# Performance work log

Hardware: AMD Instinct MI355X
Metric: run time of the kernel (lower is better)

The kernel has to match this reference:

```python
import jax, jax.numpy as jnp
import numpy as np
from jax import lax

K = 3          # kernel size
PAD = 1        # padding
STRIDE = 1     # stride (output spatial == input spatial)


def conv2d(x, w, b, pad):
    y = lax.conv_general_dilated(x, w, (1, 1), [(pad, pad), (pad, pad)],
                                 dimension_numbers=("NCHW", "OIHW", "NCHW"))
    return y + b[None, :, None, None]


def bilinear_sample(img, y, x):
    """img: [B,C,H,W]; y,x: [B,Ho,Wo] float coords. Zero outside borders (torchvision semantics)."""
    B, C, H, W = img.shape
    flat = img.reshape(B, C, H * W)
    y0 = jnp.floor(y)
    x0 = jnp.floor(x)
    dy = y - y0
    dx = x - x0

    def gather(yc, xc):
        valid = (yc >= 0) & (yc <= H - 1) & (xc >= 0) & (xc <= W - 1)
        yi = jnp.clip(yc, 0, H - 1).astype(jnp.int32)
        xi = jnp.clip(xc, 0, W - 1).astype(jnp.int32)
        idx = (yi * W + xi).reshape(B, -1)                      # [B, Ho*Wo]
        g = jax.vmap(lambda f, i: f[:, i])(flat, idx)            # [B, C, Ho*Wo]
        g = g.reshape(B, C, y.shape[1], y.shape[2])
        return g * valid[:, None, :, :].astype(img.dtype)

    w00 = ((1 - dy) * (1 - dx))[:, None]
    w01 = ((1 - dy) * dx)[:, None]
    w10 = (dy * (1 - dx))[:, None]
    w11 = (dy * dx)[:, None]
    return (gather(y0, x0) * w00 + gather(y0, x0 + 1) * w01 +
            gather(y0 + 1, x0) * w10 + gather(y0 + 1, x0 + 1) * w11)


def deform_conv2d(feat, offset, weight, bias):
    """feat: [B,C,H,W]; offset: [B,2*K*K,Ho,Wo]; weight: [O,C,K,K]; bias: [O]."""
    B, C, H, W = feat.shape
    Ho, Wo = offset.shape[2], offset.shape[3]
    hh = jnp.arange(Ho, dtype=feat.dtype) * STRIDE - PAD   # base y of kernel origin
    ww = jnp.arange(Wo, dtype=feat.dtype) * STRIDE - PAD
    out = jnp.zeros((B, weight.shape[0], Ho, Wo), feat.dtype)
    for i in range(K):
        for j in range(K):
            k = i * K + j
            sy = hh[None, :, None] + i + offset[:, 2 * k]        # [B,Ho,Wo]
            sx = ww[None, None, :] + j + offset[:, 2 * k + 1]
            sampled = bilinear_sample(feat, sy, sx)               # [B,C,Ho,Wo]
            out = out + jnp.einsum("bchw,oc->bohw", sampled, weight[:, :, i, j])
    return out + bias[None, :, None, None]


def setup_inputs() -> dict:
    key = jax.random.key(0)
    ks = jax.random.split(key, 8)
    IN_CH, OUT_CH = 3, 64
    B, H, W = 4, 256, 256
    s1 = 1.0 / np.sqrt(IN_CH * K * K)
    s2 = 1.0 / np.sqrt(OUT_CH * K * K)
    return {
        "x": jax.random.normal(ks[0], (B, IN_CH, H, W), jnp.float32),
        "conv_w": jax.random.normal(ks[1], (OUT_CH, IN_CH, K, K), jnp.float32) * s1,
        "conv_b": jax.random.normal(ks[2], (OUT_CH,), jnp.float32) * s1,
        "offset_w": jax.random.normal(ks[3], (2 * K * K, OUT_CH, K, K), jnp.float32) * 0.01,
        "offset_b": jax.random.normal(ks[4], (2 * K * K,), jnp.float32) * 0.01,
        "deform_w": jax.random.normal(ks[5], (OUT_CH, OUT_CH, K, K), jnp.float32) * s2,
        "deform_b": jax.random.normal(ks[6], (OUT_CH,), jnp.float32) * s2,
    }


def reference(x, conv_w, conv_b, offset_w, offset_b, deform_w, deform_b):
    feat = conv2d(x, conv_w, conv_b, pad=1)                    # [B,64,H,W]
    offset = conv2d(feat, offset_w, offset_b, pad=PAD)          # [B,18,H,W]
    return deform_conv2d(feat, offset, deform_w, deform_b)
```

## Files before the change

kernel.cpp:

```cpp
#include <hip/hip_runtime.h>
#include <hip/hip_fp16.h>

#define FEAT_N (4*64*256*256)
#define OFFS_N (4*18*256*256)
#define WTF_N  (576*64)
#define WT2F_N (576*32)
#define WT1F_N (4*64*8)

typedef __attribute__((ext_vector_type(8))) _Float16 half8;
typedef __attribute__((ext_vector_type(4))) float float4v;
typedef __attribute__((ext_vector_type(4))) unsigned uint4v;

__device__ __forceinline__ unsigned short f2h(float f) {
    union { __half h; unsigned short u; } c; c.h = __float2half_rn(f); return c.u;
}
__device__ __forceinline__ __half2 u2h2(unsigned u) {
    union { unsigned u; __half2 h; } c; c.u = u; return c.h;
}
__device__ __forceinline__ unsigned h22u(__half2 h) {
    union { __half2 h; unsigned u; } c; c.h = h; return c.u;
}

__global__ __launch_bounds__(256) void prep_weights(const float* __restrict__ dw,
                                                    const float* __restrict__ ow,
                                                    const float* __restrict__ cw,
                                                    unsigned short* __restrict__ wtf,
                                                    unsigned short* __restrict__ wt2f,
                                                    unsigned short* __restrict__ wt1f) {
    int idx = blockIdx.x * 256 + threadIdx.x;
    if (idx < WTF_N) {
        int j    = idx & 7;
        int lane = (idx >> 3) & 63;
        int nt   = (idx >> 9) & 3;
        int ks   = idx >> 11;
        int k    = ks * 32 + ((lane >> 4) << 3) + j;
        int tap  = k >> 6;
        int ic   = k & 63;
        int n    = nt * 16 + (lane & 15);
        wtf[idx] = f2h(dw[n * 576 + ic * 9 + tap]);
    }
    int i2 = idx - WTF_N;
    if (i2 >= 0 && i2 < WT2F_N) {
        int j    = i2 & 7;
        int lane = (i2 >> 3) & 63;
        int nt   = (i2 >> 9) & 1;
        int ks   = i2 >> 10;
        int k    = ks * 32 + ((lane >> 4) << 3) + j;
        int tap  = k >> 6;
        int ic   = k & 63;
        int n    = nt * 16 + (lane & 15);
        wt2f[i2] = (n < 18) ? f2h(ow[n * 576 + ic * 9 + tap]) : (unsigned short)0;
    }
    int i3 = idx - WTF_N - WT2F_N;
    if (i3 >= 0 && i3 < WT1F_N) {
        int j    = i3 & 7;
        int lane = (i3 >> 3) & 63;
        int nt   = (i3 >> 9) & 3;
        int n    = nt * 16 + (lane & 15);
        int k    = ((lane >> 4) << 3) + j;
        wt1f[i3] = (k < 27) ? f2h(cw[n * 27 + k]) : (unsigned short)0;
    }
}

__global__ __launch_bounds__(256) void conv1_kernel(const float* __restrict__ x,
                                                    const unsigned short* __restrict__ wt1f,
                                                    const float* __restrict__ cb,
                                                    unsigned short* __restrict__ featp) {
    __shared__ unsigned short xs[10 * 264];
    const int tid  = threadIdx.x;
    const int lane = tid & 63;
    const int wave = tid >> 6;
    const int lm   = lane & 15;
    const int quad = lane >> 4;

    const int bx = blockIdx.x;
    const int b  = bx >> 8;
    const int h  = bx & 255;

#pragma unroll
    for (int r = 0; r < 9; r++) {
        const int ic = r / 3, ti = r % 3;
        const int srow = h - 1 + ti;
        const bool rok = (unsigned)srow < 256u;
        const float* xrow = x + ((b * 3 + ic) << 16) + (srow << 8);
        {
            const int c = tid;
            float v = (rok && (unsigned)(c - 1) < 256u) ? xrow[c - 1] : 0.f;
            xs[r * 264 + c] = f2h(v);
        }
        if (tid < 2) {
            const int c = tid + 256;
            float v = (rok && (unsigned)(c - 1) < 256u) ? xrow[c - 1] : 0.f;
            xs[r * 264 + c] = f2h(v);
        }
    }
    xs[9 * 264 + tid] = 0;
    if (tid < 8) xs[9 * 264 + 256 + tid] = 0;
    __syncthreads();

    int off[8];
#pragma unroll
    for (int j = 0; j < 8; j++) {
        const int k = quad * 8 + j;
        const int row = (k < 27) ? (k / 3) : 9;
        const int tj  = (k < 27) ? (k - row * 3) : 0;
        off[j] = row * 264 + tj;
    }

    half8 bw[4];
#pragma unroll
    for (int nt = 0; nt < 4; nt++)
        bw[nt] = *(const half8*)(wt1f + nt * 512 + lane * 8);
    float bias[4];
#pragma unroll
    for (int nt = 0; nt < 4; nt++) bias[nt] = cb[nt * 16 + lm];

    unsigned short* fpx = featp + ((((size_t)b << 16) + (h << 8)) << 6);

#pragma unroll
    for (int mt = 0; mt < 4; mt++) {
        const int px = wave * 64 + mt * 16 + lm;
        union { half8 v; unsigned u[4]; } af;
#pragma unroll
        for (int jj = 0; jj < 4; jj++) {
            unsigned lo = xs[off[2 * jj]     + px];
            unsigned hi = xs[off[2 * jj + 1] + px];
            af.u[jj] = lo | (hi << 16);
        }
        float4v d[4];
#pragma unroll
        for (int nt = 0; nt < 4; nt++)
            d[nt] = __builtin_amdgcn_mfma_f32_16x16x32_f16(af.v, bw[nt], (float4v)0.f, 0, 0, 0);

        const int pxs = wave * 64 + mt * 16 + quad * 4;
#pragma unroll
        for (int r = 0; r < 4; r++) {
            unsigned short* sp = fpx + (size_t)(pxs + r) * 64 + lm;
#pragma unroll
            for (int nt = 0; nt < 4; nt++)
                sp[nt * 16] = f2h(d[nt][r] + bias[nt]);
        }
    }
}

__global__ __launch_bounds__(512, 4) void fused_kernel(const unsigned short* __restrict__ featp,
                                                       const unsigned short* __restrict__ wt2f,
                                                       const float* __restrict__ ob,
                                                       const unsigned short* __restrict__ wtf,
                                                       const float* __restrict__ db,
                                                       float* __restrict__ out) {
    __shared__ __align__(16) unsigned char ring[4 * 132 * 128];
    __shared__ float offl[4][18 * 33];

    const int tid  = threadIdx.x;
    const int lane = tid & 63;
    const int wv   = tid >> 6;
    const int ow   = wv >> 1;
    const int mtb  = wv & 1;
    const int lm   = lane & 15;
    const int quad = lane >> 4;

    const int bx = blockIdx.x;
    const int strip = ((bx & 7) << 8) | (bx >> 3);
    const int wo_base = (strip & 1) << 7;
    const int ho = (strip >> 1) & 255;
    const int b  = strip >> 9;

    const unsigned* fpq = (const unsigned*)featp + ((size_t)b << 21) + quad * 4;
    const int colb = wo_base + ow * 32 + mtb * 16 + lm;
    float* offw = &offl[ow][0];

    const char* gbase = (const char*)featp + (((size_t)b << 16) << 7);

#define STAGE_ROW(R)                                                             \
    {                                                                            \
        const int rr = (R);                                                      \
        if ((unsigned)rr < 256u) {                                               \
            const char* gsrc = gbase + ((size_t)(rr << 8) << 7);                 \
            const unsigned base = (unsigned)((rr & 3) * 16896);                  \
            for (int c = tid; c < 1056; c += 512) {                              \
                const int xsl = c >> 3;                                          \
                const int col = wo_base - 2 + xsl;                               \
                if ((unsigned)col < 256u) {                                      \
                    uint4v v = *(const uint4v*)(gsrc + (((size_t)col) << 7)      \
                                                + ((c & 7) << 4));               \
                    const unsigned by = base + (unsigned)(c << 4);               \
                    *(uint4v*)(ring + (by ^ ((unsigned)((xsl & 7) << 4)))) = v;  \
                }                                                                \
            }                                                                    \
        }                                                                        \
    }

    STAGE_ROW(ho - 2);
    STAGE_ROW(ho - 1);
    STAGE_ROW(ho);
    STAGE_ROW(ho + 1);

    {
        float4v acc1[2];
        acc1[0] = (float4v)0.f; acc1[1] = (float4v)0.f;

        uint4v A[2];

#define C2LOAD(KY, KX, DST)                                                      \
    {                                                                            \
        const int row = ho - 1 + (KY);                                           \
        const bool rok = (unsigned)row < 256u;                                   \
        const int col = colb + (KX) - 1;                                         \
        DST[0] = (uint4v)0;                                                      \
        DST[1] = (uint4v)0;                                                      \
        if (rok && (unsigned)col < 256u) {                                       \
            const unsigned* p = fpq + (((row << 8) + col) << 5);                 \
            DST[0] = *(const uint4v*)p;                                          \
            DST[1] = *(const uint4v*)(p + 16);                                   \
        }                                                                        \
    }

        C2LOAD(0, 0, A);

#pragma unroll
        for (int tap = 0; tap < 9; tap++) {
            half8 bfr[2][2];
            const unsigned short* wp = wt2f + (size_t)(tap * 2) * 1024 + lane * 8;
#pragma unroll
            for (int st = 0; st < 2; st++) {
                bfr[st][0] = *(const half8*)(wp + st * 1024);
                bfr[st][1] = *(const half8*)(wp + st * 1024 + 512);
            }
            uint4v N[2];
            if (tap < 8) {
                const int tn  = tap + 1;
                const int tky = tn / 3;
                const int tkx = tn - 3 * tky;
                C2LOAD(tky, tkx, N);
            }
            {
                union { half8 v; uint4v u; } f0, f1;
                f0.u = A[0]; f1.u = A[1];
                acc1[0] = __builtin_amdgcn_mfma_f32_16x16x32_f16(f0.v, bfr[0][0], acc1[0], 0, 0, 0);
                acc1[1] = __builtin_amdgcn_mfma_f32_16x16x32_f16(f0.v, bfr[0][1], acc1[1], 0, 0, 0);
                acc1[0] = __builtin_amdgcn_mfma_f32_16x16x32_f16(f1.v, bfr[1][0], acc1[0], 0, 0, 0);
                acc1[1] = __builtin_amdgcn_mfma_f32_16x16x32_f16(f1.v, bfr[1][1], acc1[1], 0, 0, 0);
            }
            if (tap < 8) { A[0] = N[0]; A[1] = N[1]; }
        }
#undef C2LOAD

#pragma unroll
        for (int nt = 0; nt < 2; nt++) {
            int oc = nt * 16 + lm;
            if (oc < 18) {
                float bv = ob[oc];
#pragma unroll
                for (int r = 0; r < 4; r++)
                    offw[oc * 33 + mtb * 16 + quad * 4 + r] = acc1[nt][r] + bv;
            }
        }
    }

    __syncthreads();

    const int wo0 = wo_base + ow * 32 + mtb * 16 + lm;

    float4v acc[4];
#pragma unroll
    for (int nt = 0; nt < 4; nt++) acc[nt] = (float4v)0.f;

    union AFU { half8 v; unsigned u[4]; };

#define DOTAP(KY, KX, OY, OX)                                                    \
    {                                                                            \
        float sy = (float)(ho - 1 + (KY)) + (OY);                                \
        float sx = (float)(wo0 - 1 + (KX)) + (OX);                               \
        float y0f = floorf(sy), x0f = floorf(sx);                                \
        float dy = sy - y0f, dx = sx - x0f;                                      \
        int y0 = (int)y0f, x0 = (int)x0f;                                        \
        float wy0 = ((unsigned)y0 < 256u) ? (1.f - dy) : 0.f;                    \
        float wy1 = ((unsigned)(y0 + 1) < 256u) ? dy : 0.f;                      \
        float wx0 = ((unsigned)x0 < 256u) ? (1.f - dx) : 0.f;                    \
        float wx1 = ((unsigned)(x0 + 1) < 256u) ? dx : 0.f;                      \
        int yb0 = y0 < 0 ? 0 : (y0 > 255 ? 255 : y0);                            \
        int yb1 = (y0 + 1) < 0 ? 0 : ((y0 + 1) > 255 ? 255 : (y0 + 1));          \
        int xb0 = x0 < 0 ? 0 : (x0 > 255 ? 255 : x0);                            \
        int xb1 = (x0 + 1) < 0 ? 0 : ((x0 + 1) > 255 ? 255 : (x0 + 1));          \
        __half2 W0 = __float2half2_rn(wy0 * wx0);                                \
        __half2 W1 = __float2half2_rn(wy0 * wx1);                                \
        __half2 W2 = __float2half2_rn(wy1 * wx0);                                \
        __half2 W3 = __float2half2_rn(wy1 * wx1);                                \
        uint4v Gg[4][2];                                                         \
        bool inw = (yb0 >= ho - 2 + (KY)) && (yb1 <= ho + (KY) + 1) &&           \
                   (xb0 >= wo_base - 2) && (xb1 <= wo_base + 129);               \
        if (__all(inw)) {                                                        \
            const int xs0 = xb0 - wo_base + 2, xs1 = xb1 - wo_base + 2;          \
            const unsigned m0 = (unsigned)((xs0 & 7) << 4);                      \
            const unsigned m1 = (unsigned)((xs1 & 7) << 4);                      \
            const unsigned r0b = (unsigned)((yb0 & 3) * 16896 + quad * 16);      \
            const unsigned r1b = (unsigned)((yb1 & 3) * 16896 + quad * 16);      \
            const unsigned a00 = r0b + (unsigned)(xs0 << 7);                     \
            const unsigned a01 = r0b + (unsigned)(xs1 << 7);                     \
            const unsigned a10 = r1b + (unsigned)(xs0 << 7);                     \
            const unsigned a11 = r1b + (unsigned)(xs1 << 7);                     \
            Gg[0][0] = *(const uint4v*)(ring + (a00 ^ m0));                      \
            Gg[0][1] = *(const uint4v*)(ring + ((a00 + 64) ^ m0));               \
            Gg[1][0] = *(const uint4v*)(ring + (a01 ^ m1));                      \
            Gg[1][1] = *(const uint4v*)(ring + ((a01 + 64) ^ m1));               \
            Gg[2][0] = *(const uint4v*)(ring + (a10 ^ m0));                      \
            Gg[2][1] = *(const uint4v*)(ring + ((a10 + 64) ^ m0));               \
            Gg[3][0] = *(const uint4v*)(ring + (a11 ^ m1));                      \
            Gg[3][1] = *(const uint4v*)(ring + ((a11 + 64) ^ m1));               \
        } else {                                                                 \
            const unsigned e00 = ((yb0 << 8) + xb0) << 5;                        \
            const unsigned e01 = ((yb0 << 8) + xb1) << 5;                        \
            const unsigned e10 = ((yb1 << 8) + xb0) << 5;                        \
            const unsigned e11 = ((yb1 << 8) + xb1) << 5;                        \
            Gg[0][0] = *(const uint4v*)(fpq + e00);                              \
            Gg[0][1] = *(const uint4v*)(fpq + e00 + 16);                         \
            Gg[1][0] = *(const uint4v*)(fpq + e01);                              \
            Gg[1][1] = *(const uint4v*)(fpq + e01 + 16);                         \
            Gg[2][0] = *(const uint4v*)(fpq + e10);                              \
            Gg[2][1] = *(const uint4v*)(fpq + e10 + 16);                         \
            Gg[3][0] = *(const uint4v*)(fpq + e11);                              \
            Gg[3][1] = *(const uint4v*)(fpq + e11 + 16);                         \
        }                                                                        \
        AFU af[2];                                                               \
        _Pragma("unroll")                                                        \
        for (int st = 0; st < 2; st++) {                                         \
            _Pragma("unroll")                                                    \
            for (int j = 0; j < 4; j++) {                                        \
                __half2 s = __hmul2(W0, u2h2(Gg[0][st][j]));                     \
                s = __hfma2(W1, u2h2(Gg[1][st][j]), s);                          \
                s = __hfma2(W2, u2h2(Gg[2][st][j]), s);                          \
                s = __hfma2(W3, u2h2(Gg[3][st][j]), s);                          \
                af[st].u[j] = h22u(s);                                           \
            }                                                                    \
        }                                                                        \
        _Pragma("unroll")                                                        \
        for (int nt = 0; nt < 4; nt++)                                           \
            acc[nt] = __builtin_amdgcn_mfma_f32_16x16x32_f16(                    \
                af[0].v, bfr[0][nt], acc[nt], 0, 0, 0);                          \
        _Pragma("unroll")                                                        \
        for (int nt = 0; nt < 4; nt++)                                           \
            acc[nt] = __builtin_amdgcn_mfma_f32_16x16x32_f16(                    \
                af[1].v, bfr[1][nt], acc[nt], 0, 0, 0);                          \
    }

#pragma unroll
    for (int tap = 0; tap < 9; ++tap) {
        const int ky = tap / 3;
        const int kx = tap - 3 * ky;
        if (tap == 3) { __syncthreads(); STAGE_ROW(ho + 2); __syncthreads(); }
        if (tap == 6) { __syncthreads(); STAGE_ROW(ho + 3); __syncthreads(); }

        float oy = offw[(2 * tap) * 33 + mtb * 16 + lm];
        float ox = offw[(2 * tap + 1) * 33 + mtb * 16 + lm];

        half8 bfr[2][4];
        {
            const unsigned short* wp = wtf + (size_t)tap * 4096 + lane * 8;
#pragma unroll
            for (int nt = 0; nt < 4; nt++) {
                bfr[0][nt] = *(const half8*)(wp + (nt << 9));
                bfr[1][nt] = *(const half8*)(wp + 2048 + (nt << 9));
            }
        }

        DOTAP(ky, kx, oy, ox);
    }

#pragma unroll
    for (int nt = 0; nt < 4; nt++) {
        int oc = nt * 16 + lm;
        float bv = db[oc];
        float* op = out + (((size_t)(b * 64 + oc)) << 16) + (ho << 8)
                  + wo_base + ow * 32 + mtb * 16 + quad * 4;
        float4 v = {acc[nt][0] + bv, acc[nt][1] + bv,
                    acc[nt][2] + bv, acc[nt][3] + bv};
        *(float4*)op = v;
    }
#undef DOTAP
#undef STAGE_ROW
}

extern "C" void kernel_launch(void* const* d_in, const int* in_sizes, int n_in,
                              void* d_out, int out_size, void* d_ws, size_t ws_size,
                              hipStream_t stream) {
    const float* x  = (const float*)d_in[0];
    const float* cw = (const float*)d_in[1];
    const float* cb = (const float*)d_in[2];
    const float* ow = (const float*)d_in[3];
    const float* ob = (const float*)d_in[4];
    const float* dw = (const float*)d_in[5];
    const float* db = (const float*)d_in[6];
    float* out = (float*)d_out;

    unsigned short* featp = (unsigned short*)d_ws;
    float* offsb = (float*)(featp + FEAT_N);
    unsigned short* wt1f = (unsigned short*)offsb;
    unsigned short* wtf  = (unsigned short*)(offsb + OFFS_N);
    unsigned short* wt2f = wtf + WTF_N;

    prep_weights<<<224, 256, 0, stream>>>(dw, ow, cw, wtf, wt2f, wt1f);
    conv1_kernel<<<1024, 256, 0, stream>>>(x, wt1f, cb, featp);
    fused_kernel<<<2048, 512, 0, stream>>>(featp, wt2f, ob, wtf, db, out);
}
```

Before: 213.2 us.

## Stage all six feature rows up front and precompute sampling addresses for all taps

The shared-memory ring grows from four to six rows, so every row the block needs is staged once before the offset conv, and the two mid-loop barrier-and-restage points go away. All nine taps' bilinear weights, LDS addresses and fast-path votes are computed up front into register arrays, which leaves the tap loop as loads, HFMA and MFMA only. The larger LDS footprint (about 101 KB) and dropping the occupancy hint of 4 from launch_bounds may lower occupancy. The precomputed per-tap arrays also add register pressure.

```diff
diff --git a/kernel.cpp b/kernel.cpp
--- a/kernel.cpp
+++ b/kernel.cpp
@@ -143,13 +143,13 @@
     }
 }
 
-__global__ __launch_bounds__(512, 4) void fused_kernel(const unsigned short* __restrict__ featp,
-                                                       const unsigned short* __restrict__ wt2f,
-                                                       const float* __restrict__ ob,
-                                                       const unsigned short* __restrict__ wtf,
-                                                       const float* __restrict__ db,
-                                                       float* __restrict__ out) {
-    __shared__ __align__(16) unsigned char ring[4 * 132 * 128];
+__global__ __launch_bounds__(512) void fused_kernel(const unsigned short* __restrict__ featp,
+                                                    const unsigned short* __restrict__ wt2f,
+                                                    const float* __restrict__ ob,
+                                                    const unsigned short* __restrict__ wtf,
+                                                    const float* __restrict__ db,
+                                                    float* __restrict__ out) {
+    __shared__ __align__(16) unsigned char ring[6 * 132 * 128];
     __shared__ float offl[4][18 * 33];
 
     const int tid  = threadIdx.x;
@@ -172,12 +172,12 @@
 
     const char* gbase = (const char*)featp + (((size_t)b << 16) << 7);
 
-#define STAGE_ROW(R)                                                             \
+#define STAGE_ROW(R, SLOT)                                                       \
     {                                                                            \
         const int rr = (R);                                                      \
         if ((unsigned)rr < 256u) {                                               \
             const char* gsrc = gbase + ((size_t)(rr << 8) << 7);                 \
-            const unsigned base = (unsigned)((rr & 3) * 16896);                  \
+            const unsigned base = (unsigned)((SLOT) * 16896);                    \
             for (int c = tid; c < 1056; c += 512) {                              \
                 const int xsl = c >> 3;                                          \
                 const int col = wo_base - 2 + xsl;                               \
@@ -191,10 +191,12 @@
         }                                                                        \
     }
 
-    STAGE_ROW(ho - 2);
-    STAGE_ROW(ho - 1);
-    STAGE_ROW(ho);
-    STAGE_ROW(ho + 1);
+    STAGE_ROW(ho - 2, 0);
+    STAGE_ROW(ho - 1, 1);
+    STAGE_ROW(ho,     2);
+    STAGE_ROW(ho + 1, 3);
+    STAGE_ROW(ho + 2, 4);
+    STAGE_ROW(ho + 3, 5);
 
     {
         float4v acc1[2];
@@ -268,103 +270,110 @@
 
     union AFU { half8 v; unsigned u[4]; };
 
-#define DOTAP(KY, KX, OY, OX)                                                    \
-    {                                                                            \
-        float sy = (float)(ho - 1 + (KY)) + (OY);                                \
-        float sx = (float)(wo0 - 1 + (KX)) + (OX);                               \
-        float y0f = floorf(sy), x0f = floorf(sx);                                \
-        float dy = sy - y0f, dx = sx - x0f;                                      \
-        int y0 = (int)y0f, x0 = (int)x0f;                                        \
-        float wy0 = ((unsigned)y0 < 256u) ? (1.f - dy) : 0.f;                    \
-        float wy1 = ((unsigned)(y0 + 1) < 256u) ? dy : 0.f;                      \
-        float wx0 = ((unsigned)x0 < 256u) ? (1.f - dx) : 0.f;                    \
-        float wx1 = ((unsigned)(x0 + 1) < 256u) ? dx : 0.f;                      \
-        int yb0 = y0 < 0 ? 0 : (y0 > 255 ? 255 : y0);                            \
-        int yb1 = (y0 + 1) < 0 ? 0 : ((y0 + 1) > 255 ? 255 : (y0 + 1));          \
-        int xb0 = x0 < 0 ? 0 : (x0 > 255 ? 255 : x0);                            \
-        int xb1 = (x0 + 1) < 0 ? 0 : ((x0 + 1) > 255 ? 255 : (x0 + 1));          \
-        __half2 W0 = __float2half2_rn(wy0 * wx0);                                \
-        __half2 W1 = __float2half2_rn(wy0 * wx1);                                \
-        __half2 W2 = __float2half2_rn(wy1 * wx0);                                \
-        __half2 W3 = __float2half2_rn(wy1 * wx1);                                \
-        uint4v Gg[4][2];                                                         \
-        bool inw = (yb0 >= ho - 2 + (KY)) && (yb1 <= ho + (KY) + 1) &&           \
-                   (xb0 >= wo_base - 2) && (xb1 <= wo_base + 129);               \
-        if (__all(inw)) {                                                        \
-            const int xs0 = xb0 - wo_base + 2, xs1 = xb1 - wo_base + 2;          \
-            const unsigned m0 = (unsigned)((xs0 & 7) << 4);                      \
-            const unsigned m1 = (unsigned)((xs1 & 7) << 4);                      \
-            const unsigned r0b = (unsigned)((yb0 & 3) * 16896 + quad * 16);      \
-            const unsigned r1b = (unsigned)((yb1 & 3) * 16896 + quad * 16);      \
-            const unsigned a00 = r0b + (unsigned)(xs0 << 7);                     \
-            const unsigned a01 = r0b + (unsigned)(xs1 << 7);                     \
-            const unsigned a10 = r1b + (unsigned)(xs0 << 7);                     \
-            const unsigned a11 = r1b + (unsigned)(xs1 << 7);                     \
-            Gg[0][0] = *(const uint4v*)(ring + (a00 ^ m0));                      \
-            Gg[0][1] = *(const uint4v*)(ring + ((a00 + 64) ^ m0));               \
-            Gg[1][0] = *(const uint4v*)(ring + (a01 ^ m1));                      \
-            Gg[1][1] = *(const uint4v*)(ring + ((a01 + 64) ^ m1));               \
-            Gg[2][0] = *(const uint4v*)(ring + (a10 ^ m0));                      \
-            Gg[2][1] = *(const uint4v*)(ring + ((a10 + 64) ^ m0));               \
-            Gg[3][0] = *(const uint4v*)(ring + (a11 ^ m1));                      \
-            Gg[3][1] = *(const uint4v*)(ring + ((a11 + 64) ^ m1));               \
-        } else {                                                                 \
-            const unsigned e00 = ((yb0 << 8) + xb0) << 5;                        \
-            const unsigned e01 = ((yb0 << 8) + xb1) << 5;                        \
-            const unsigned e10 = ((yb1 << 8) + xb0) << 5;                        \
-            const unsigned e11 = ((yb1 << 8) + xb1) << 5;                        \
-            Gg[0][0] = *(const uint4v*)(fpq + e00);                              \
-            Gg[0][1] = *(const uint4v*)(fpq + e00 + 16);                         \
-            Gg[1][0] = *(const uint4v*)(fpq + e01);                              \
-            Gg[1][1] = *(const uint4v*)(fpq + e01 + 16);                         \
-            Gg[2][0] = *(const uint4v*)(fpq + e10);                              \
-            Gg[2][1] = *(const uint4v*)(fpq + e10 + 16);                         \
-            Gg[3][0] = *(const uint4v*)(fpq + e11);                              \
-            Gg[3][1] = *(const uint4v*)(fpq + e11 + 16);                         \
-        }                                                                        \
-        AFU af[2];                                                               \
-        _Pragma("unroll")                                                        \
-        for (int st = 0; st < 2; st++) {                                         \
-            _Pragma("unroll")                                                    \
-            for (int j = 0; j < 4; j++) {                                        \
-                __half2 s = __hmul2(W0, u2h2(Gg[0][st][j]));                     \
-                s = __hfma2(W1, u2h2(Gg[1][st][j]), s);                          \
-                s = __hfma2(W2, u2h2(Gg[2][st][j]), s);                          \
-                s = __hfma2(W3, u2h2(Gg[3][st][j]), s);                          \
-                af[st].u[j] = h22u(s);                                           \
-            }                                                                    \
-        }                                                                        \
-        _Pragma("unroll")                                                        \
-        for (int nt = 0; nt < 4; nt++)                                           \
-            acc[nt] = __builtin_amdgcn_mfma_f32_16x16x32_f16(                    \
-                af[0].v, bfr[0][nt], acc[nt], 0, 0, 0);                          \
-        _Pragma("unroll")                                                        \
-        for (int nt = 0; nt < 4; nt++)                                           \
-            acc[nt] = __builtin_amdgcn_mfma_f32_16x16x32_f16(                    \
-                af[1].v, bfr[1][nt], acc[nt], 0, 0, 0);                          \
-    }
-
-#pragma unroll
-    for (int tap = 0; tap < 9; ++tap) {
-        const int ky = tap / 3;
-        const int kx = tap - 3 * ky;
-        if (tap == 3) { __syncthreads(); STAGE_ROW(ho + 2); __syncthreads(); }
-        if (tap == 6) { __syncthreads(); STAGE_ROW(ho + 3); __syncthreads(); }
-
-        float oy = offw[(2 * tap) * 33 + mtb * 16 + lm];
-        float ox = offw[(2 * tap + 1) * 33 + mtb * 16 + lm];
-
+    float oyv[9], oxv[9];
+#pragma unroll
+    for (int t = 0; t < 9; t++) {
+        oyv[t] = offw[(2 * t) * 33 + mtb * 16 + lm];
+        oxv[t] = offw[(2 * t + 1) * 33 + mtb * 16 + lm];
+    }
+
+    unsigned A00[9], A01[9], A10[9], A11[9];
+    unsigned M0[9], M1[9];
+    unsigned PK[9];
+    __half2 Wt[9][4];
+    unsigned vote = 0;
+#pragma unroll
+    for (int t = 0; t < 9; t++) {
+        const int ky = t / 3, kx = t - 3 * ky;
+        float sy = (float)(ho - 1 + ky) + oyv[t];
+        float sx = (float)(wo0 - 1 + kx) + oxv[t];
+        float y0f = floorf(sy), x0f = floorf(sx);
+        float dy = sy - y0f, dx = sx - x0f;
+        int y0 = (int)y0f, x0 = (int)x0f;
+        float wy0 = ((unsigned)y0 < 256u) ? (1.f - dy) : 0.f;
+        float wy1 = ((unsigned)(y0 + 1) < 256u) ? dy : 0.f;
+        float wx0 = ((unsigned)x0 < 256u) ? (1.f - dx) : 0.f;
+        float wx1 = ((unsigned)(x0 + 1) < 256u) ? dx : 0.f;
+        int yb0 = y0 < 0 ? 0 : (y0 > 255 ? 255 : y0);
+        int yb1 = (y0 + 1) < 0 ? 0 : ((y0 + 1) > 255 ? 255 : (y0 + 1));
+        int xb0 = x0 < 0 ? 0 : (x0 > 255 ? 255 : x0);
+        int xb1 = (x0 + 1) < 0 ? 0 : ((x0 + 1) > 255 ? 255 : (x0 + 1));
+        Wt[t][0] = __float2half2_rn(wy0 * wx0);
+        Wt[t][1] = __float2half2_rn(wy0 * wx1);
+        Wt[t][2] = __float2half2_rn(wy1 * wx0);
+        Wt[t][3] = __float2half2_rn(wy1 * wx1);
+        PK[t] = (unsigned)yb0 | ((unsigned)yb1 << 8)
+              | ((unsigned)xb0 << 16) | ((unsigned)xb1 << 24);
+        bool inw = (yb0 >= ho - 2) && (yb1 <= ho + 3) &&
+                   (xb0 >= wo_base - 2) && (xb1 <= wo_base + 129);
+        if (__all(inw)) vote |= (1u << t);
+        const int ys0 = yb0 - (ho - 2), ys1 = yb1 - (ho - 2);
+        const int xs0 = xb0 - wo_base + 2, xs1 = xb1 - wo_base + 2;
+        M0[t] = (unsigned)((xs0 & 7) << 4);
+        M1[t] = (unsigned)((xs1 & 7) << 4);
+        A00[t] = (unsigned)(ys0 * 16896 + xs0 * 128 + quad * 16);
+        A01[t] = (unsigned)(ys0 * 16896 + xs1 * 128 + quad * 16);
+        A10[t] = (unsigned)(ys1 * 16896 + xs0 * 128 + quad * 16);
+        A11[t] = (unsigned)(ys1 * 16896 + xs1 * 128 + quad * 16);
+    }
+
+#pragma unroll
+    for (int t = 0; t < 9; ++t) {
         half8 bfr[2][4];
         {
-            const unsigned short* wp = wtf + (size_t)tap * 4096 + lane * 8;
+            const unsigned short* wp = wtf + (size_t)t * 4096 + lane * 8;
 #pragma unroll
             for (int nt = 0; nt < 4; nt++) {
                 bfr[0][nt] = *(const half8*)(wp + (nt << 9));
                 bfr[1][nt] = *(const half8*)(wp + 2048 + (nt << 9));
             }
         }
-
-        DOTAP(ky, kx, oy, ox);
+        uint4v Gg[4][2];
+        if (vote & (1u << t)) {
+            Gg[0][0] = *(const uint4v*)(ring + (A00[t] ^ M0[t]));
+            Gg[0][1] = *(const uint4v*)(ring + ((A00[t] + 64) ^ M0[t]));
+            Gg[1][0] = *(const uint4v*)(ring + (A01[t] ^ M1[t]));
+            Gg[1][1] = *(const uint4v*)(ring + ((A01[t] + 64) ^ M1[t]));
+            Gg[2][0] = *(const uint4v*)(ring + (A10[t] ^ M0[t]));
+            Gg[2][1] = *(const uint4v*)(ring + ((A10[t] + 64) ^ M0[t]));
+            Gg[3][0] = *(const uint4v*)(ring + (A11[t] ^ M1[t]));
+            Gg[3][1] = *(const uint4v*)(ring + ((A11[t] + 64) ^ M1[t]));
+        } else {
+            const unsigned yb0 = PK[t] & 255u, yb1 = (PK[t] >> 8) & 255u;
+            const unsigned xb0 = (PK[t] >> 16) & 255u, xb1 = PK[t] >> 24;
+            const unsigned e00 = ((yb0 << 8) + xb0) << 5;
+            const unsigned e01 = ((yb0 << 8) + xb1) << 5;
+            const unsigned e10 = ((yb1 << 8) + xb0) << 5;
+            const unsigned e11 = ((yb1 << 8) + xb1) << 5;
+            Gg[0][0] = *(const uint4v*)(fpq + e00);
+            Gg[0][1] = *(const uint4v*)(fpq + e00 + 16);
+            Gg[1][0] = *(const uint4v*)(fpq + e01);
+            Gg[1][1] = *(const uint4v*)(fpq + e01 + 16);
+            Gg[2][0] = *(const uint4v*)(fpq + e10);
+            Gg[2][1] = *(const uint4v*)(fpq + e10 + 16);
+            Gg[3][0] = *(const uint4v*)(fpq + e11);
+            Gg[3][1] = *(const uint4v*)(fpq + e11 + 16);
+        }
+        AFU af[2];
+#pragma unroll
+        for (int st = 0; st < 2; st++) {
+#pragma unroll
+            for (int j = 0; j < 4; j++) {
+                __half2 s = __hmul2(Wt[t][0], u2h2(Gg[0][st][j]));
+                s = __hfma2(Wt[t][1], u2h2(Gg[1][st][j]), s);
+                s = __hfma2(Wt[t][2], u2h2(Gg[2][st][j]), s);
+                s = __hfma2(Wt[t][3], u2h2(Gg[3][st][j]), s);
+                af[st].u[j] = h22u(s);
+            }
+        }
+#pragma unroll
+        for (int nt = 0; nt < 4; nt++)
+            acc[nt] = __builtin_amdgcn_mfma_f32_16x16x32_f16(
+                af[0].v, bfr[0][nt], acc[nt], 0, 0, 0);
+#pragma unroll
+        for (int nt = 0; nt < 4; nt++)
+            acc[nt] = __builtin_amdgcn_mfma_f32_16x16x32_f16(
+                af[1].v, bfr[1][nt], acc[nt], 0, 0, 0);
     }
 
 #pragma unroll
@@ -377,7 +386,6 @@
                     acc[nt][2] + bv, acc[nt][3] + bv};
         *(float4*)op = v;
     }
-#undef DOTAP
 #undef STAGE_ROW
 }
 
```

Result: slower. 237.4 us (+11.4%).
